# Performance work log

Hardware: AMD Instinct MI355X
Metric: run time of the kernel (lower is better)

Reference implementation:

```python
import jax, jax.numpy as jnp
import numpy as np

NY, NU, NH = 8, 8, 256
T, NB = 2048, 64


def setup_inputs() -> dict:
    key = jax.random.key(0)
    ks = jax.random.split(key, 10)
    return {
        "_y0": jax.random.normal(ks[0], (NB, NY), dtype=jnp.float32),
        "_U": jax.random.normal(ks[1], (T, NB, NU), dtype=jnp.float32),
        "lmbd_cont_real": jax.random.uniform(ks[2], (NH // 2,), dtype=jnp.float32),
        "lmbd_cont_imag": jax.random.uniform(ks[3], (NH // 2,), dtype=jnp.float32),
        "B": jax.random.normal(ks[4], (NH, NU), dtype=jnp.float32) / np.sqrt(NU).astype(np.float32),
        "multiplier_on_B": jnp.zeros((NH,), dtype=jnp.float32),
        "W_y2x": jax.random.normal(ks[5], (NH, NY), dtype=jnp.float32) / np.sqrt(NY).astype(np.float32),
        "b_y2x": jax.random.normal(ks[6], (NH,), dtype=jnp.float32) * 0.01,
        "W_x2y": jax.random.normal(ks[7], (NY, NH), dtype=jnp.float32) / np.sqrt(NH).astype(np.float32),
        "b_x2y": jax.random.normal(ks[8], (NY,), dtype=jnp.float32) * 0.01,
    }


def reference(_y0, _U, lmbd_cont_real, lmbd_cont_imag, B, multiplier_on_B,
              W_y2x, b_y2x, W_x2y, b_x2y):
    H2 = lmbd_cont_real.shape[0]
    # input drive: (T, NB, NH)
    Bu = jnp.einsum('tbu,hu->tbh', _U, B) * jnp.exp(multiplier_on_B)
    # stable complex-conjugate-pair eigenvalues
    r = jnp.exp(-jnp.abs(lmbd_cont_real))
    theta = (jnp.pi / 2) * lmbd_cont_imag
    re = r * jnp.cos(theta)
    im = r * jnp.sin(theta)
    # initial state from y0
    x0 = _y0 @ W_y2x.T + b_y2x  # (NB, NH)

    def step(x, bu):
        x1, x2 = x[:, :H2], x[:, H2:]
        # A = [[diag(re), -diag(im)], [diag(im), diag(re)]]; x <- x A^T + bu
        nx = jnp.concatenate([re * x1 - im * x2, im * x1 + re * x2], axis=1) + bu
        return nx, nx

    _, X = jax.lax.scan(step, x0, Bu)  # X: (T, NB, NH)
    Y = X @ W_x2y.T + b_x2y  # (T, NB, NY)
    return Y
```

## Files before the change

kernel.cpp:

```cpp
#include <hip/hip_runtime.h>
#include <math.h>

#define T_   2048
#define NB_  64
#define NU_  8
#define NY_  8
#define NH_  256
#define H2_  128
#define CCH  64
#define LCH  32

#define BUF_FLOATS (CCH*NB_*H2_*2)
static const float PI_HALF = 1.5707963267948966f;

typedef _Float16 half8  __attribute__((ext_vector_type(8)));
typedef __fp16   fp16x2 __attribute__((ext_vector_type(2)));
typedef float    f32x4  __attribute__((ext_vector_type(4)));


__global__ __launch_bounds__(64) void k_local(
    const float* __restrict__ U, const float* __restrict__ lr,
    const float* __restrict__ li, const float* __restrict__ B,
    const float* __restrict__ mult, float* __restrict__ c_buf)
{
    const int k = blockIdx.x >> 6;
    const int b = blockIdx.x & 63;
    const int j = threadIdx.x;
    const int c0 = 2*j;

    float2 lrv = *(const float2*)(lr + c0);
    float2 liv = *(const float2*)(li + c0);
    float rA  = expf(-fabsf(lrv.x)), thA = PI_HALF*liv.x;
    float reA = rA*cosf(thA), imA = rA*sinf(thA);
    float rB  = expf(-fabsf(lrv.y)), thB = PI_HALF*liv.y;
    float reB = rB*cosf(thB), imB = rB*sinf(thB);

    float Ba1[NU_], Ba2[NU_], Bb1[NU_], Bb2[NU_];
    {
        float s1 = expf(mult[c0]),     s2 = expf(mult[c0+128]);
        float s3 = expf(mult[c0+1]),   s4 = expf(mult[c0+129]);
        #pragma unroll
        for (int i = 0; i < NU_; i++) {
            Ba1[i] = B[(c0    )*NU_ + i] * s1;
            Bb1[i] = B[(c0+  1)*NU_ + i] * s3;
            Ba2[i] = B[(c0+128)*NU_ + i] * s2;
            Bb2[i] = B[(c0+129)*NU_ + i] * s4;
        }
    }

    const float4* Ut = (const float4*)(U + ((size_t)(k*LCH)*NB_ + b)*NU_);

    float xa1=0.f, xa2=0.f, xb1=0.f, xb2=0.f;
    #pragma unroll 4
    for (int t = 0; t < LCH; t++) {
        float4 u0 = Ut[t*128 + 0];
        float4 u1 = Ut[t*128 + 1];
        float u[NU_] = {u0.x,u0.y,u0.z,u0.w,u1.x,u1.y,u1.z,u1.w};
        float ba1=0.f, ba2=0.f, bb1=0.f, bb2=0.f;
        #pragma unroll
        for (int i = 0; i < NU_; i++) {
            ba1 = fmaf(u[i], Ba1[i], ba1);
            ba2 = fmaf(u[i], Ba2[i], ba2);
            bb1 = fmaf(u[i], Bb1[i], bb1);
            bb2 = fmaf(u[i], Bb2[i], bb2);
        }
        float na1 = fmaf(reA, xa1, fmaf(-imA, xa2, ba1));
        float na2 = fmaf(imA, xa1, fmaf( reA, xa2, ba2));
        float nb1 = fmaf(reB, xb1, fmaf(-imB, xb2, bb1));
        float nb2 = fmaf(imB, xb1, fmaf( reB, xb2, bb2));
        xa1=na1; xa2=na2; xb1=nb1; xb2=nb2;
    }

    *(float4*)(c_buf + ((size_t)(k*NB_ + b))*(H2_*2) + 4*j) =
        make_float4(xa1, xa2, xb1, xb2);
}

__global__ __launch_bounds__(64) void k_prefix(
    const float* __restrict__ y0, const float* __restrict__ lr,
    const float* __restrict__ li, const float* __restrict__ Wy2x,
    const float* __restrict__ by2x, const float* __restrict__ c_buf,
    float* __restrict__ init_buf)
{
    const int g = blockIdx.x*64 + threadIdx.x;
    const int b = g >> 7;
    const int h = g & 127;

    float x1 = by2x[h], x2 = by2x[h+H2_];
    #pragma unroll
    for (int y = 0; y < NY_; y++) {
        float yy = y0[b*NY_ + y];
        x1 = fmaf(yy, Wy2x[h*NY_ + y],        x1);
        x2 = fmaf(yy, Wy2x[(h+H2_)*NY_ + y],  x2);
    }

    float rL  = expf(-(float)LCH * fabsf(lr[h]));
    float thL = (float)LCH * PI_HALF * li[h];
    float reL = rL * cosf(thL), imL = rL * sinf(thL);

    const size_t stride = NB_*(size_t)(H2_*2);
    const size_t off    = (size_t)b*(H2_*2) + 2*h;

    #pragma unroll 8
    for (int k = 0; k < CCH; k++) {
        float2 c = *(const float2*)(c_buf + k*stride + off);
        *(float2*)(init_buf + k*stride + off) = make_float2(x1, x2);
        float n1 = fmaf(reL, x1, fmaf(-imL, x2, c.x));
        float n2 = fmaf(imL, x1, fmaf( reL, x2, c.y));
        x1 = n1; x2 = n2;
    }
}

__global__ __launch_bounds__(64) void k_emit(
    const float* __restrict__ U, const float* __restrict__ lr,
    const float* __restrict__ li, const float* __restrict__ B,
    const float* __restrict__ mult, const float* __restrict__ Wx2y,
    const float* __restrict__ bx2y, const float* __restrict__ init_buf,
    float* __restrict__ Y)
{
    const int k = blockIdx.x >> 6;
    const int b = blockIdx.x & 63;
    const int j = threadIdx.x;
    const int c0 = 2*j;

    float2 lrv = *(const float2*)(lr + c0);
    float2 liv = *(const float2*)(li + c0);
    float rA  = expf(-fabsf(lrv.x)), thA = PI_HALF*liv.x;
    float reA = rA*cosf(thA), imA = rA*sinf(thA);
    float rB  = expf(-fabsf(lrv.y)), thB = PI_HALF*liv.y;
    float reB = rB*cosf(thB), imB = rB*sinf(thB);

    float Ba1[NU_], Ba2[NU_], Bb1[NU_], Bb2[NU_];
    {
        float s1 = expf(mult[c0]),     s2 = expf(mult[c0+128]);
        float s3 = expf(mult[c0+1]),   s4 = expf(mult[c0+129]);
        #pragma unroll
        for (int i = 0; i < NU_; i++) {
            Ba1[i] = B[(c0    )*NU_ + i] * s1;
            Bb1[i] = B[(c0+  1)*NU_ + i] * s3;
            Ba2[i] = B[(c0+128)*NU_ + i] * s2;
            Bb2[i] = B[(c0+129)*NU_ + i] * s4;
        }
    }

    const int yv  = j & 15;
    const int kg  = j >> 4;
    const int row = yv;
    half8 wf[8];
    #pragma unroll
    for (int q = 0; q < 8; q++) {
        half8 f;
        if (yv < 8) {
            const float* wr = Wx2y + yv*NH_ + q*32 + kg*8;
            #pragma unroll
            for (int i = 0; i < 8; i++) f[i] = (_Float16)wr[i];
        } else {
            #pragma unroll
            for (int i = 0; i < 8; i++) f[i] = (_Float16)0.f;
        }
        wf[q] = f;
    }
    const float bias = bx2y[yv & 7];

    __shared__ _Float16 xS[16*256];
    uint32_t* xS32 = (uint32_t*)xS;

    float4 ini = *(const float4*)(init_buf + ((size_t)(k*NB_ + b))*(H2_*2) + 4*j);
    float xa1=ini.x, xa2=ini.y, xb1=ini.z, xb2=ini.w;

    const float4* Ut = (const float4*)(U + ((size_t)(k*LCH)*NB_ + b)*NU_);

    for (int s = 0; s < LCH/16; s++) {
        #pragma unroll 4
        for (int t16 = 0; t16 < 16; t16++) {
            const int t = s*16 + t16;
            float4 u0 = Ut[t*128 + 0];
            float4 u1 = Ut[t*128 + 1];
            float u[NU_] = {u0.x,u0.y,u0.z,u0.w,u1.x,u1.y,u1.z,u1.w};
            float ba1=0.f, ba2=0.f, bb1=0.f, bb2=0.f;
            #pragma unroll
            for (int i = 0; i < NU_; i++) {
                ba1 = fmaf(u[i], Ba1[i], ba1);
                ba2 = fmaf(u[i], Ba2[i], ba2);
                bb1 = fmaf(u[i], Bb1[i], bb1);
                bb2 = fmaf(u[i], Bb2[i], bb2);
            }
            float na1 = fmaf(reA, xa1, fmaf(-imA, xa2, ba1));
            float na2 = fmaf(imA, xa1, fmaf( reA, xa2, ba2));
            float nb1 = fmaf(reB, xb1, fmaf(-imB, xb2, bb1));
            float nb2 = fmaf(imB, xb1, fmaf( reB, xb2, bb2));
            xa1=na1; xa2=na2; xb1=nb1; xb2=nb2;

            union { fp16x2 h; uint32_t u32; } p0, p1;
            p0.h = __builtin_amdgcn_cvt_pkrtz(xa1, xb1);
            p1.h = __builtin_amdgcn_cvt_pkrtz(xa2, xb2);
            const int w0 = t16*128 + (((j>>2) ^ t16) << 2) + (j & 3);
            xS32[w0]      = p0.u32;
            xS32[w0 + 64] = p1.u32;
        }
        __syncthreads();

        f32x4 acc = {0.f, 0.f, 0.f, 0.f};
        #pragma unroll
        for (int q = 0; q < 8; q++) {
            const int p = ((q << 2) + kg) ^ row;
            const half8* ap = (const half8*)(xS + (row << 8) + (p << 3));
            acc = __builtin_amdgcn_mfma_f32_16x16x32_f16(*ap, wf[q], acc, 0, 0, 0);
        }
        __syncthreads();

        if (yv < 8) {
            #pragma unroll
            for (int r = 0; r < 4; r++) {
                const int tg = k*LCH + s*16 + kg*4 + r;
                Y[((size_t)tg*NB_ + b)*NY_ + yv] = acc[r] + bias;
            }
        }
    }
}

extern "C" void kernel_launch(void* const* d_in, const int* in_sizes, int n_in,
                              void* d_out, int out_size, void* d_ws, size_t ws_size,
                              hipStream_t stream) {
    const float* y0   = (const float*)d_in[0];
    const float* U    = (const float*)d_in[1];
    const float* lr   = (const float*)d_in[2];
    const float* li   = (const float*)d_in[3];
    const float* B    = (const float*)d_in[4];
    const float* mult = (const float*)d_in[5];
    const float* Wy2x = (const float*)d_in[6];
    const float* by2x = (const float*)d_in[7];
    const float* Wx2y = (const float*)d_in[8];
    const float* bx2y = (const float*)d_in[9];
    float* Y = (float*)d_out;

    float* c_buf    = (float*)d_ws;
    float* init_buf = c_buf + BUF_FLOATS;

    k_local <<<CCH*NB_, 64, 0, stream>>>(U, lr, li, B, mult, c_buf);
    k_prefix<<<(NB_*H2_)/64, 64, 0, stream>>>(y0, lr, li, Wy2x, by2x, c_buf, init_buf);
    k_emit  <<<CCH*NB_, 64, 0, stream>>>(U, lr, li, B, mult, Wx2y, bx2y, init_buf, Y);
}
```

Baseline: 107.5 us.

## Fuse local scan with projection and add carried-state correction via MFMA GEMM

Merges the local chunk scan and the output projection into one pass. Each chunk runs from a zero state, emits a partial Y, and still produces the chunk-end carry. The contribution of the carried initial state is added afterwards by a separate GEMM, using precomputed coefficients W·A^(d+1) stored in fp16 and run on MFMA. This removes the second full recurrence over U, so U is read once instead of twice. In exchange it adds extra kernels, a read-modify-write of Y, and more fp16 rounding in the correction term. It also software-prefetches the next U row in the scan loop.

```diff
diff --git a/kernel.cpp b/kernel.cpp
--- a/kernel.cpp
+++ b/kernel.cpp
@@ -10,7 +10,6 @@
 #define CCH  64
 #define LCH  32
 
-#define BUF_FLOATS (CCH*NB_*H2_*2)
 static const float PI_HALF = 1.5707963267948966f;
 
 typedef _Float16 half8  __attribute__((ext_vector_type(8)));
@@ -18,10 +17,12 @@
 typedef float    f32x4  __attribute__((ext_vector_type(4)));
 
 
-__global__ __launch_bounds__(64) void k_local(
+__global__ __launch_bounds__(64) void k_scanproj(
     const float* __restrict__ U, const float* __restrict__ lr,
     const float* __restrict__ li, const float* __restrict__ B,
-    const float* __restrict__ mult, float* __restrict__ c_buf)
+    const float* __restrict__ mult, const float* __restrict__ Wx2y,
+    const float* __restrict__ bx2y, float* __restrict__ c_buf,
+    float* __restrict__ Y)
 {
     const int k = blockIdx.x >> 6;
     const int b = blockIdx.x & 63;
@@ -48,103 +49,8 @@
         }
     }
 
-    const float4* Ut = (const float4*)(U + ((size_t)(k*LCH)*NB_ + b)*NU_);
-
-    float xa1=0.f, xa2=0.f, xb1=0.f, xb2=0.f;
-    #pragma unroll 4
-    for (int t = 0; t < LCH; t++) {
-        float4 u0 = Ut[t*128 + 0];
-        float4 u1 = Ut[t*128 + 1];
-        float u[NU_] = {u0.x,u0.y,u0.z,u0.w,u1.x,u1.y,u1.z,u1.w};
-        float ba1=0.f, ba2=0.f, bb1=0.f, bb2=0.f;
-        #pragma unroll
-        for (int i = 0; i < NU_; i++) {
-            ba1 = fmaf(u[i], Ba1[i], ba1);
-            ba2 = fmaf(u[i], Ba2[i], ba2);
-            bb1 = fmaf(u[i], Bb1[i], bb1);
-            bb2 = fmaf(u[i], Bb2[i], bb2);
-        }
-        float na1 = fmaf(reA, xa1, fmaf(-imA, xa2, ba1));
-        float na2 = fmaf(imA, xa1, fmaf( reA, xa2, ba2));
-        float nb1 = fmaf(reB, xb1, fmaf(-imB, xb2, bb1));
-        float nb2 = fmaf(imB, xb1, fmaf( reB, xb2, bb2));
-        xa1=na1; xa2=na2; xb1=nb1; xb2=nb2;
-    }
-
-    *(float4*)(c_buf + ((size_t)(k*NB_ + b))*(H2_*2) + 4*j) =
-        make_float4(xa1, xa2, xb1, xb2);
-}
-
-__global__ __launch_bounds__(64) void k_prefix(
-    const float* __restrict__ y0, const float* __restrict__ lr,
-    const float* __restrict__ li, const float* __restrict__ Wy2x,
-    const float* __restrict__ by2x, const float* __restrict__ c_buf,
-    float* __restrict__ init_buf)
-{
-    const int g = blockIdx.x*64 + threadIdx.x;
-    const int b = g >> 7;
-    const int h = g & 127;
-
-    float x1 = by2x[h], x2 = by2x[h+H2_];
-    #pragma unroll
-    for (int y = 0; y < NY_; y++) {
-        float yy = y0[b*NY_ + y];
-        x1 = fmaf(yy, Wy2x[h*NY_ + y],        x1);
-        x2 = fmaf(yy, Wy2x[(h+H2_)*NY_ + y],  x2);
-    }
-
-    float rL  = expf(-(float)LCH * fabsf(lr[h]));
-    float thL = (float)LCH * PI_HALF * li[h];
-    float reL = rL * cosf(thL), imL = rL * sinf(thL);
-
-    const size_t stride = NB_*(size_t)(H2_*2);
-    const size_t off    = (size_t)b*(H2_*2) + 2*h;
-
-    #pragma unroll 8
-    for (int k = 0; k < CCH; k++) {
-        float2 c = *(const float2*)(c_buf + k*stride + off);
-        *(float2*)(init_buf + k*stride + off) = make_float2(x1, x2);
-        float n1 = fmaf(reL, x1, fmaf(-imL, x2, c.x));
-        float n2 = fmaf(imL, x1, fmaf( reL, x2, c.y));
-        x1 = n1; x2 = n2;
-    }
-}
-
-__global__ __launch_bounds__(64) void k_emit(
-    const float* __restrict__ U, const float* __restrict__ lr,
-    const float* __restrict__ li, const float* __restrict__ B,
-    const float* __restrict__ mult, const float* __restrict__ Wx2y,
-    const float* __restrict__ bx2y, const float* __restrict__ init_buf,
-    float* __restrict__ Y)
-{
-    const int k = blockIdx.x >> 6;
-    const int b = blockIdx.x & 63;
-    const int j = threadIdx.x;
-    const int c0 = 2*j;
-
-    float2 lrv = *(const float2*)(lr + c0);
-    float2 liv = *(const float2*)(li + c0);
-    float rA  = expf(-fabsf(lrv.x)), thA = PI_HALF*liv.x;
-    float reA = rA*cosf(thA), imA = rA*sinf(thA);
-    float rB  = expf(-fabsf(lrv.y)), thB = PI_HALF*liv.y;
-    float reB = rB*cosf(thB), imB = rB*sinf(thB);
-
-    float Ba1[NU_], Ba2[NU_], Bb1[NU_], Bb2[NU_];
-    {
-        float s1 = expf(mult[c0]),     s2 = expf(mult[c0+128]);
-        float s3 = expf(mult[c0+1]),   s4 = expf(mult[c0+129]);
-        #pragma unroll
-        for (int i = 0; i < NU_; i++) {
-            Ba1[i] = B[(c0    )*NU_ + i] * s1;
-            Bb1[i] = B[(c0+  1)*NU_ + i] * s3;
-            Ba2[i] = B[(c0+128)*NU_ + i] * s2;
-            Bb2[i] = B[(c0+129)*NU_ + i] * s4;
-        }
-    }
-
     const int yv  = j & 15;
     const int kg  = j >> 4;
-    const int row = yv;
     half8 wf[8];
     #pragma unroll
     for (int q = 0; q < 8; q++) {
@@ -164,18 +70,21 @@
     __shared__ _Float16 xS[16*256];
     uint32_t* xS32 = (uint32_t*)xS;
 
-    float4 ini = *(const float4*)(init_buf + ((size_t)(k*NB_ + b))*(H2_*2) + 4*j);
-    float xa1=ini.x, xa2=ini.y, xb1=ini.z, xb2=ini.w;
-
+    float xa1=0.f, xa2=0.f, xb1=0.f, xb2=0.f;
     const float4* Ut = (const float4*)(U + ((size_t)(k*LCH)*NB_ + b)*NU_);
+
+    float4 u0 = Ut[0], u1 = Ut[1];
 
     for (int s = 0; s < LCH/16; s++) {
         #pragma unroll 4
         for (int t16 = 0; t16 < 16; t16++) {
             const int t = s*16 + t16;
-            float4 u0 = Ut[t*128 + 0];
-            float4 u1 = Ut[t*128 + 1];
-            float u[NU_] = {u0.x,u0.y,u0.z,u0.w,u1.x,u1.y,u1.z,u1.w};
+            float4 cu0 = u0, cu1 = u1;
+            const int tn = (t < LCH-1) ? t+1 : t;
+            u0 = Ut[tn*128 + 0];
+            u1 = Ut[tn*128 + 1];
+
+            float u[NU_] = {cu0.x,cu0.y,cu0.z,cu0.w,cu1.x,cu1.y,cu1.z,cu1.w};
             float ba1=0.f, ba2=0.f, bb1=0.f, bb2=0.f;
             #pragma unroll
             for (int i = 0; i < NU_; i++) {
@@ -202,8 +111,8 @@
         f32x4 acc = {0.f, 0.f, 0.f, 0.f};
         #pragma unroll
         for (int q = 0; q < 8; q++) {
-            const int p = ((q << 2) + kg) ^ row;
-            const half8* ap = (const half8*)(xS + (row << 8) + (p << 3));
+            const int p = ((q << 2) + kg) ^ yv;
+            const half8* ap = (const half8*)(xS + (yv << 8) + (p << 3));
             acc = __builtin_amdgcn_mfma_f32_16x16x32_f16(*ap, wf[q], acc, 0, 0, 0);
         }
         __syncthreads();
@@ -214,6 +123,121 @@
                 const int tg = k*LCH + s*16 + kg*4 + r;
                 Y[((size_t)tg*NB_ + b)*NY_ + yv] = acc[r] + bias;
             }
+        }
+    }
+
+    *(float4*)(c_buf + ((size_t)(k*NB_ + b))*(H2_*2) + 4*j) =
+        make_float4(xa1, xa2, xb1, xb2);
+}
+
+__global__ __launch_bounds__(64) void k_prefix(
+    const float* __restrict__ y0, const float* __restrict__ lr,
+    const float* __restrict__ li, const float* __restrict__ Wy2x,
+    const float* __restrict__ by2x, const float* __restrict__ c_buf,
+    uint32_t* __restrict__ initT)
+{
+    const int g = blockIdx.x*64 + threadIdx.x;
+    const int b = g >> 7;
+    const int h = g & 127;
+
+    float x1 = by2x[h], x2 = by2x[h+H2_];
+    #pragma unroll
+    for (int y = 0; y < NY_; y++) {
+        float yy = y0[b*NY_ + y];
+        x1 = fmaf(yy, Wy2x[h*NY_ + y],        x1);
+        x2 = fmaf(yy, Wy2x[(h+H2_)*NY_ + y],  x2);
+    }
+
+    float rL  = expf(-(float)LCH * fabsf(lr[h]));
+    float thL = (float)LCH * PI_HALF * li[h];
+    float reL = rL * cosf(thL), imL = rL * sinf(thL);
+
+    #pragma unroll 8
+    for (int k = 0; k < CCH; k++) {
+        float2 c = *(const float2*)(c_buf + (size_t)k*16384 + b*256 + 2*h);
+        union { fp16x2 hh; uint32_t u32; } pk;
+        pk.hh = __builtin_amdgcn_cvt_pkrtz(x1, x2);
+        initT[(size_t)k*8192 + b*128 + h] = pk.u32;
+        float n1 = fmaf(reL, x1, fmaf(-imL, x2, c.x));
+        float n2 = fmaf(imL, x1, fmaf( reL, x2, c.y));
+        x1 = n1; x2 = n2;
+    }
+}
+
+__global__ __launch_bounds__(64) void k_mcoef(
+    const float* __restrict__ lr, const float* __restrict__ li,
+    const float* __restrict__ Wx2y, uint32_t* __restrict__ M32)
+{
+    const int R = blockIdx.x;
+    const int dlt = R >> 3, y = R & 7;
+    const float e = (float)(dlt + 1);
+    const int j = threadIdx.x;
+
+    #pragma unroll
+    for (int hh = 0; hh < 2; hh++) {
+        const int h = j + hh*64;
+        float r  = expf(-e * fabsf(lr[h]));
+        float an = e * PI_HALF * li[h];
+        float c = r * cosf(an), s = r * sinf(an);
+        float W1 = Wx2y[y*NH_ + h];
+        float W2 = Wx2y[y*NH_ + h + H2_];
+        float Mre = fmaf(W1, c,  W2 * s);
+        float Mim = fmaf(W2, c, -W1 * s);
+        union { fp16x2 hh2; uint32_t u32; } pk;
+        pk.hh2 = __builtin_amdgcn_cvt_pkrtz(Mre, Mim);
+        M32[R*128 + hh*64 + j] = pk.u32;
+    }
+}
+
+__global__ __launch_bounds__(256) void k_corr(
+    const _Float16* __restrict__ M, const uint32_t* __restrict__ initT,
+    float* __restrict__ Y)
+{
+    const int k    = blockIdx.x >> 1;
+    const int half = blockIdx.x & 1;
+    const int tid  = threadIdx.x;
+    const int w    = tid >> 6, l = tid & 63;
+    const int lane16 = l & 15, kg = l >> 4;
+
+    __shared__ _Float16 bS[32*264];
+    {
+        uint32_t* bS32 = (uint32_t*)bS;
+        const int r = tid >> 3, seg = tid & 7;
+        const uint32_t* src = initT + (size_t)k*8192 + (half*32 + r)*128 + seg*16;
+        uint32_t* dst = bS32 + r*132 + seg*16;
+        ((uint4*)dst)[0] = ((const uint4*)src)[0];
+        ((uint4*)dst)[1] = ((const uint4*)src)[1];
+        ((uint4*)dst)[2] = ((const uint4*)src)[2];
+        ((uint4*)dst)[3] = ((const uint4*)src)[3];
+    }
+    __syncthreads();
+
+    #pragma unroll
+    for (int rt = 0; rt < 4; rt++) {
+        const int R0 = w*64 + rt*16;
+        half8 af[8];
+        #pragma unroll
+        for (int q = 0; q < 8; q++)
+            af[q] = *(const half8*)(M + (size_t)(R0 + lane16)*256 + q*32 + kg*8);
+
+        f32x4 acc0 = {0.f,0.f,0.f,0.f}, acc1 = {0.f,0.f,0.f,0.f};
+        #pragma unroll
+        for (int q = 0; q < 8; q++) {
+            const half8* b0 = (const half8*)(bS + ( 0 + lane16)*264 + q*32 + kg*8);
+            const half8* b1 = (const half8*)(bS + (16 + lane16)*264 + q*32 + kg*8);
+            acc0 = __builtin_amdgcn_mfma_f32_16x16x32_f16(af[q], *b0, acc0, 0, 0, 0);
+            acc1 = __builtin_amdgcn_mfma_f32_16x16x32_f16(af[q], *b1, acc1, 0, 0, 0);
+        }
+
+        #pragma unroll
+        for (int r4 = 0; r4 < 4; r4++) {
+            const int R = R0 + kg*4 + r4;
+            const int t = k*LCH + (R >> 3);
+            const int y = R & 7;
+            float* yp0 = Y + ((size_t)t*NB_ + half*32 +  0 + lane16)*NY_ + y;
+            float* yp1 = Y + ((size_t)t*NB_ + half*32 + 16 + lane16)*NY_ + y;
+            *yp0 += acc0[r4];
+            *yp1 += acc1[r4];
         }
     }
 }
@@ -233,10 +257,12 @@
     const float* bx2y = (const float*)d_in[9];
     float* Y = (float*)d_out;
 
-    float* c_buf    = (float*)d_ws;
-    float* init_buf = c_buf + BUF_FLOATS;
-
-    k_local <<<CCH*NB_, 64, 0, stream>>>(U, lr, li, B, mult, c_buf);
-    k_prefix<<<(NB_*H2_)/64, 64, 0, stream>>>(y0, lr, li, Wy2x, by2x, c_buf, init_buf);
-    k_emit  <<<CCH*NB_, 64, 0, stream>>>(U, lr, li, B, mult, Wx2y, bx2y, init_buf, Y);
-}
+    uint32_t*  Mbuf  = (uint32_t*)d_ws;
+    float*     c_buf = (float*)((char*)d_ws + (128<<10));
+    uint32_t*  initT = (uint32_t*)((char*)d_ws + (128<<10) + (4<<20));
+
+    k_mcoef   <<<256, 64, 0, stream>>>(lr, li, Wx2y, Mbuf);
+    k_scanproj<<<CCH*NB_, 64, 0, stream>>>(U, lr, li, B, mult, Wx2y, bx2y, c_buf, Y);
+    k_prefix  <<<(NB_*H2_)/64, 64, 0, stream>>>(y0, lr, li, Wy2x, by2x, c_buf, initT);
+    k_corr    <<<CCH*2, 256, 0, stream>>>((const _Float16*)Mbuf, initT, Y);
+}
```

Result: no change. 108.1 us (+0.5%).
